# Kernel optimization log

Hardware: AMD Instinct MI355X
Metric: run time of the kernel (lower is better)

## Reference

```python
import jax, jax.numpy as jnp
import numpy as np

DIM = 256
QK = 256
HEADS = 8
NWIN = 16
TOPK = 4
MLP_RATIO = 4
SCALE = QK ** -0.5


def setup_inputs() -> dict:
    key = jax.random.key(0)
    ks = jax.random.split(key, 8)
    p = lambda k, shp: jax.random.normal(k, shp, jnp.float32) * 0.02
    hid = MLP_RATIO * DIM
    return {
        "x": jax.random.normal(ks[0], (8, DIM, 64, 64), jnp.float32),
        # to_q / to_kv : 1x1 Conv2d_BN (eval-mode BN with running stats 0/1 -> scale+shift)
        "wq": p(ks[1], (QK, DIM)), "gq": jnp.ones((QK,), jnp.float32), "bq": jnp.zeros((QK,), jnp.float32),
        "wkv": p(ks[2], (QK + DIM, DIM)), "gkv": jnp.ones((QK + DIM,), jnp.float32), "bkv": jnp.zeros((QK + DIM,), jnp.float32),
        # LEPE depthwise 5x5 conv
        "w_lepe": p(ks[3], (DIM, 1, 5, 5)), "b_lepe": jnp.zeros((DIM,), jnp.float32),
        # Mlp: fc1(1x1 Conv2d_BN) -> dwconv3x3 -> ReLU -> fc2(1x1 Conv2d_BN)
        "w_fc1": p(ks[4], (hid, DIM)), "g_fc1": jnp.ones((hid,), jnp.float32), "b_fc1": jnp.zeros((hid,), jnp.float32),
        "w_dw": p(ks[5], (hid, 1, 3, 3)), "b_dw": jnp.zeros((hid,), jnp.float32),
        "w_fc2": p(ks[6], (DIM, hid)), "g_fc2": jnp.ones((DIM,), jnp.float32), "b_fc2": jnp.zeros((DIM,), jnp.float32),
    }


def _dwconv(x, w, b, pad):
    # x: NCHW, w: (C,1,k,k) depthwise
    out = jax.lax.conv_general_dilated(
        x, w, (1, 1), [(pad, pad), (pad, pad)],
        feature_group_count=x.shape[1],
        dimension_numbers=("NCHW", "OIHW", "NCHW"))
    return out + b[None, :, None, None]


def _bra(x, wq, gq, bq, wkv, gkv, bkv, w_lepe, b_lepe):
    # Bi-Level Routing Attention. x: NCHW
    N, C, H, W = x.shape
    j = i = NWIN
    h, w_ = H // j, W // i          # per-window spatial (4,4)
    p2, w2 = j * i, h * w_          # 256 windows, 16 tokens/window
    xh = x.transpose(0, 2, 3, 1)    # NHWC
    # windowize: (N, p2, h, w, C)
    xw = xh.reshape(N, j, h, i, w_, C).transpose(0, 1, 3, 2, 4, 5).reshape(N, p2, h, w_, C)
    # 1x1 conv + BN(eval: stats 0/1) == matmul * gamma + beta
    q = (xw @ wq.T) * gq + bq                    # (N,p2,h,w,QK)
    kv = (xw @ wkv.T) * gkv + bkv                # (N,p2,h,w,QK+C)
    q_pix = q.reshape(N, p2, w2, QK)
    kv_pix = kv.reshape(N, p2, w2, QK + C)       # identity kv_down
    q_win = q.mean((2, 3))                       # (N,p2,QK)
    k_win = kv[..., :QK].mean((2, 3))            # (N,p2,QK)
    # LEPE on V in full-image layout
    v_img = kv[..., QK:].reshape(N, j, i, h, w_, C).transpose(0, 1, 3, 2, 4, 5).reshape(N, H, W, C)
    lepe = _dwconv(v_img.transpose(0, 3, 1, 2), w_lepe, b_lepe, 2).transpose(0, 2, 3, 1)  # NHWC
    # window-level topk routing (detached, non-differentiable)
    qd = jax.lax.stop_gradient(q_win)
    kd = jax.lax.stop_gradient(k_win)
    logit = (qd * SCALE) @ kd.transpose(0, 2, 1)            # (N,p2,p2)
    _, r_idx = jax.lax.top_k(logit, TOPK)                   # (N,p2,TOPK); r_weight unused (mul_weight='none')
    # gather selected KV windows: (N,p2,TOPK,w2,QK+C)
    kv_sel = jax.vmap(lambda kvp, idx: kvp[idx])(kv_pix, r_idx)
    ch_k, ch_v = QK // HEADS, C // HEADS
    k_sel = kv_sel[..., :QK].reshape(N, p2, TOPK * w2, HEADS, ch_k).transpose(0, 1, 3, 2, 4)
    v_sel = kv_sel[..., QK:].reshape(N, p2, TOPK * w2, HEADS, ch_v).transpose(0, 1, 3, 2, 4)
    qh = q_pix.reshape(N, p2, w2, HEADS, ch_k).transpose(0, 1, 3, 2, 4)
    attn = jax.nn.softmax(jnp.einsum("npmqc,npmkc->npmqk", qh * SCALE, k_sel), axis=-1)
    out = jnp.einsum("npmqk,npmkc->npmqc", attn, v_sel)     # (N,p2,HEADS,w2,ch_v)
    out = out.transpose(0, 1, 3, 2, 4).reshape(N, j, i, h, w_, C)
    out = out.transpose(0, 1, 3, 2, 4, 5).reshape(N, H, W, C)
    out = out + lepe                                         # wo = Identity
    return out.transpose(0, 3, 1, 2)                         # NCHW


def reference(x, wq, gq, bq, wkv, gkv, bkv, w_lepe, b_lepe,
              w_fc1, g_fc1, b_fc1, w_dw, b_dw, w_fc2, g_fc2, b_fc2):
    # top_Block: x = x + attn(x); x = x + mlp(x)   (drop_path inactive in eval)
    x = x + _bra(x, wq, gq, bq, wkv, gkv, bkv, w_lepe, b_lepe)
    h1 = jnp.einsum("nchw,dc->ndhw", x, w_fc1) * g_fc1[None, :, None, None] + b_fc1[None, :, None, None]
    h1 = jax.nn.relu(_dwconv(h1, w_dw, b_dw, 1))
    h2 = jnp.einsum("nchw,dc->ndhw", h1, w_fc2) * g_fc2[None, :, None, None] + b_fc2[None, :, None, None]
    return x + h2
```

## Files before the change

kernel.cpp:

```cpp
#include <hip/hip_runtime.h>
#include <hip/hip_bf16.h>

#define NBATCH 8
#define CDIM 256
#define HH 64
#define WW 64
#define HWSZ 4096
#define TT 32768
#define QKVD 768
#define TOPK 4
#define HID 1024
#define ATTN_SCALE 0.0625f

typedef __hip_bfloat16 bf16;
typedef __attribute__((ext_vector_type(8))) short s8v;
typedef __attribute__((ext_vector_type(4))) float f4v;

__device__ __forceinline__ float toF(bf16 v) { return __bfloat162float(v); }
__device__ __forceinline__ bf16  toB(float v) { return __float2bfloat16(v); }

__device__ __forceinline__ void gload_lds16(const bf16* g, bf16* l) {
    __builtin_amdgcn_global_load_lds(
        (const __attribute__((address_space(1))) void*)g,
        (__attribute__((address_space(3))) void*)l, 16, 0, 0);
}

__global__ void k_prep(const float* __restrict__ wq, const float* __restrict__ gq,
                       const float* __restrict__ wkv, const float* __restrict__ gkv,
                       const float* __restrict__ wfc1, const float* __restrict__ gfc1,
                       const float* __restrict__ wfc2, const float* __restrict__ gfc2,
                       const float* __restrict__ bq, const float* __restrict__ bkv,
                       const float* __restrict__ w_dw, const float* __restrict__ b_dw,
                       bf16* __restrict__ wbqkv, bf16* __restrict__ wbfc1,
                       bf16* __restrict__ wbfc2, float* __restrict__ bias768,
                       float* __restrict__ wdwT) {
    int i = blockIdx.x * 256 + threadIdx.x;
    if (i < 196608) {
        int r = i >> 8;
        float g = (r < 256) ? gq[r] : gkv[r - 256];
        float w = (r < 256) ? wq[i] : wkv[i - 65536];
        wbqkv[i] = toB(w * g);
        if (i < 768) bias768[i] = (i < 256) ? bq[i] : bkv[i - 256];
    } else if (i < 458752) {
        int j = i - 196608;
        wbfc1[j] = toB(wfc1[j] * gfc1[j >> 8]);
    } else if (i < 720896) {
        int j = i - 458752;
        wbfc2[j] = toB(wfc2[j] * gfc2[j >> 10]);
    } else if (i < 731136) {
        int j = i - 720896;
        int cg = j / 80, r = j - cg * 80;
        wdwT[j] = (r < 72) ? w_dw[(cg * 8 + (r & 7)) * 9 + (r >> 3)]
                           : b_dw[cg * 8 + (r - 72)];
    }
}

__global__ void k_xt(const float* __restrict__ x, bf16* __restrict__ xt) {
    __shared__ float tile[32][33];
    int s0 = blockIdx.x * 32, c0 = blockIdx.y * 32, n = blockIdx.z;
    int tx = threadIdx.x, ty = threadIdx.y;
#pragma unroll
    for (int r = 0; r < 4; r++)
        tile[ty + r * 8][tx] = x[(size_t)n * CDIM * HWSZ + (size_t)(c0 + ty + r * 8) * HWSZ + s0 + tx];
    __syncthreads();
#pragma unroll
    for (int r = 0; r < 4; r++)
        xt[((size_t)n * HWSZ + s0 + ty + r * 8) * CDIM + c0 + tx] = toB(tile[tx][ty + r * 8]);
}

__global__ void k_xwin(const float* __restrict__ x, float* __restrict__ xwin) {
    int b = blockIdx.x;
    int n = b >> 8, c = b & 255;
    int p = threadIdx.x, wy = p >> 4, wx = p & 15;
    const float* pl = x + ((size_t)n * CDIM + c) * HWSZ;
    float s = 0.f;
#pragma unroll
    for (int dy = 0; dy < 4; dy++)
#pragma unroll
        for (int dx = 0; dx < 4; dx++)
            s += pl[(wy * 4 + dy) * WW + wx * 4 + dx];
    xwin[((size_t)(n << 8) + p) * 256 + c] = s * 0.0625f;
}

__global__ void k_qkwin(const float* __restrict__ xwin,
                        const float* __restrict__ wq, const float* __restrict__ wkv,
                        const float* __restrict__ gq, const float* __restrict__ bq,
                        const float* __restrict__ gkv, const float* __restrict__ bkv,
                        float* __restrict__ qkwin) {
    __shared__ float As[16][68];
    __shared__ float Bs[16][68];
    int m0 = blockIdx.x * 64, n0 = blockIdx.y * 64;
    int tid = threadIdx.x;
    int tx = tid & 15, ty = tid >> 4;
    float acc[4][4] = {};
    for (int k0 = 0; k0 < 256; k0 += 16) {
#pragma unroll
        for (int r = 0; r < 4; r++) {
            int lin = tid + r * 256;
            int row = lin >> 4, kk = lin & 15;
            As[kk][row] = xwin[(size_t)(m0 + row) * 256 + k0 + kk];
            int n = n0 + row;
            const float* wr = (n < 256) ? (wq + (size_t)n * 256) : (wkv + (size_t)(n - 256) * 256);
            Bs[kk][row] = wr[k0 + kk];
        }
        __syncthreads();
#pragma unroll
        for (int kk = 0; kk < 16; kk++) {
            float a[4], bb[4];
#pragma unroll
            for (int i = 0; i < 4; i++) a[i] = As[kk][tx * 4 + i];
#pragma unroll
            for (int j = 0; j < 4; j++) bb[j] = Bs[kk][ty * 4 + j];
#pragma unroll
            for (int i = 0; i < 4; i++)
#pragma unroll
                for (int j = 0; j < 4; j++) acc[i][j] += a[i] * bb[j];
        }
        __syncthreads();
    }
#pragma unroll
    for (int j = 0; j < 4; j++) {
        int n = n0 + ty * 4 + j;
        float gg = (n < 256) ? gq[n] : gkv[n - 256];
        float bb = (n < 256) ? bq[n] : bkv[n - 256];
#pragma unroll
        for (int i = 0; i < 4; i++)
            qkwin[(size_t)(m0 + tx * 4 + i) * 512 + n] = acc[i][j] * gg + bb;
    }
}

__global__ void k_logits(const float* __restrict__ qkwin, float* __restrict__ logits) {
    __shared__ float As[16][68];
    __shared__ float Bs[16][68];
    int m0 = blockIdx.x * 64, n0 = blockIdx.y * 64, img = blockIdx.z;
    const float* base = qkwin + (size_t)(img << 8) * 512;
    int tid = threadIdx.x;
    int tx = tid & 15, ty = tid >> 4;
    float acc[4][4] = {};
    for (int k0 = 0; k0 < 256; k0 += 16) {
#pragma unroll
        for (int r = 0; r < 4; r++) {
            int lin = tid + r * 256;
            int row = lin >> 4, kk = lin & 15;
            As[kk][row] = base[(size_t)(m0 + row) * 512 + k0 + kk];
            Bs[kk][row] = base[(size_t)(n0 + row) * 512 + 256 + k0 + kk];
        }
        __syncthreads();
#pragma unroll
        for (int kk = 0; kk < 16; kk++) {
            float a[4], bb[4];
#pragma unroll
            for (int i = 0; i < 4; i++) a[i] = As[kk][tx * 4 + i];
#pragma unroll
            for (int j = 0; j < 4; j++) bb[j] = Bs[kk][ty * 4 + j];
#pragma unroll
            for (int i = 0; i < 4; i++)
#pragma unroll
                for (int j = 0; j < 4; j++) acc[i][j] += a[i] * bb[j];
        }
        __syncthreads();
    }
    float* Lr = logits + (size_t)(img << 8) * 256;
#pragma unroll
    for (int j = 0; j < 4; j++)
#pragma unroll
        for (int i = 0; i < 4; i++)
            Lr[(size_t)(m0 + tx * 4 + i) * 256 + n0 + ty * 4 + j] = acc[i][j];
}

__global__ __launch_bounds__(256) void k_topk(const float* __restrict__ logits,
                                              int* __restrict__ topk) {
    int row = blockIdx.x * 4 + (threadIdx.x >> 6);
    int lane = threadIdx.x & 63;
    float4 v4 = *(const float4*)(logits + (size_t)row * 256 + lane * 4);
    float v[4] = {v4.x, v4.y, v4.z, v4.w};
#pragma unroll
    for (int sel = 0; sel < TOPK; sel++) {
        float mv = v[0]; int mi = lane * 4;
#pragma unroll
        for (int j = 1; j < 4; j++)
            if (v[j] > mv) { mv = v[j]; mi = lane * 4 + j; }
#pragma unroll
        for (int off = 1; off < 64; off <<= 1) {
            float ov = __shfl_xor(mv, off);
            int oi = __shfl_xor(mi, off);
            if (ov > mv || (ov == mv && oi < mi)) { mv = ov; mi = oi; }
        }
        if (lane == 0) topk[(size_t)row * TOPK + sel] = mi;
        if ((mi >> 2) == lane) v[mi & 3] = -INFINITY;
    }
}

template <int BM, int BN>
__global__ __launch_bounds__(256) void k_mfma(const bf16* __restrict__ A,
                                              const bf16* __restrict__ Wb,
                                              const float* __restrict__ bias,
                                              bf16* __restrict__ out,
                                              int M, int N, int K) {
    constexpr int WROWS = BM / 2, WCOLS = BN / 2;
    constexpr int WM = WROWS / 16, WN = WCOLS / 16;
    constexpr int CA = (BM * 4) / 256;
    constexpr int CB = (BN * 4) / 256;
    __shared__ bf16 As[BM * 32];
    __shared__ bf16 Bs[BN * 32];
    int gx = gridDim.x;
    int lin = blockIdx.x + blockIdx.y * gx;
    int tot = gx * gridDim.y;
    int cpx = tot >> 3;
    int swz = (lin & 7) * cpx + (lin >> 3);
    int m0 = (swz % gx) * BM, n0 = (swz / gx) * BN;
    int tid = threadIdx.x;
    int w = tid >> 6, lane = tid & 63;
    int wr = w >> 1, wc = w & 1;
    int lm = lane & 15, lq = lane >> 4;
    f4v acc[WM][WN];
#pragma unroll
    for (int i = 0; i < WM; i++)
#pragma unroll
        for (int j = 0; j < WN; j++) acc[i][j] = (f4v){0.f, 0.f, 0.f, 0.f};

    for (int k0 = 0; k0 < K; k0 += 32) {
#pragma unroll
        for (int q = 0; q < CA; q++) {
            int c = tid + q * 256, row = c >> 2, col = c & 3;
            gload_lds16(A + (size_t)(m0 + row) * K + k0 + col * 8,
                        As + (size_t)(w * 64 + q * 256) * 8);
        }
#pragma unroll
        for (int q = 0; q < CB; q++) {
            int c = tid + q * 256, row = c >> 2, col = c & 3;
            gload_lds16(Wb + (size_t)(n0 + row) * K + k0 + col * 8,
                        Bs + (size_t)(w * 64 + q * 256) * 8);
        }
        asm volatile("s_waitcnt vmcnt(0)" ::: "memory");
        __syncthreads();
        s8v af[WM], bfr[WN];
#pragma unroll
        for (int i = 0; i < WM; i++)
            af[i] = *(const s8v*)&As[(wr * WROWS + i * 16 + lm) * 32 + lq * 8];
#pragma unroll
        for (int j = 0; j < WN; j++)
            bfr[j] = *(const s8v*)&Bs[(wc * WCOLS + j * 16 + lm) * 32 + lq * 8];
#pragma unroll
        for (int i = 0; i < WM; i++)
#pragma unroll
            for (int j = 0; j < WN; j++)
                acc[i][j] = __builtin_amdgcn_mfma_f32_16x16x32_bf16(af[i], bfr[j], acc[i][j], 0, 0, 0);
        __syncthreads();
    }
#pragma unroll
    for (int j = 0; j < WN; j++) {
        int n = n0 + wc * WCOLS + j * 16 + lm;
        float bb = bias[n];
#pragma unroll
        for (int i = 0; i < WM; i++) {
            int mb = m0 + wr * WROWS + i * 16 + lq * 4;
#pragma unroll
            for (int r = 0; r < 4; r++)
                out[(size_t)(mb + r) * N + n] = toB(acc[i][j][r] + bb);
        }
    }
}

__global__ __launch_bounds__(256) void k_lepe_t(const bf16* __restrict__ qkv,
                                                const float* __restrict__ w_lepe,
                                                const float* __restrict__ b_lepe,
                                                bf16* __restrict__ lepe) {
    __shared__ float lw[25 * 64 * 4];
    int tid = threadIdx.x;
    int cg = tid & 63;
    int slot = tid >> 6;
    int b = blockIdx.x;
    int n = b & 7;
    int bx = b >> 3;
    int y = bx >> 1;
    int x0 = (bx & 1) * 32 + slot * 8;
#pragma unroll
    for (int j = 0; j < 25; j++) {
        int g = tid + j * 256;
        float val = w_lepe[g];
        int ch = g / 25, k = g - ch * 25;
        lw[(k * 64 + (ch >> 2)) * 4 + (ch & 3)] = val;
    }
    float4 b4 = *(const float4*)(b_lepe + cg * 4);
    const float* bias4 = (const float*)&b4;
    __syncthreads();
    const bf16* vb = qkv + (size_t)n * HWSZ * QKVD + 512;
    bf16* dst = lepe + (size_t)n * HWSZ * CDIM;
    float o[8][4];
#pragma unroll
    for (int xi = 0; xi < 8; xi++)
#pragma unroll
        for (int c = 0; c < 4; c++) o[xi][c] = bias4[c];
#pragma unroll
    for (int dy = -2; dy <= 2; dy++) {
        int yy = y + dy;
        if (yy < 0 || yy >= HH) continue;
        float rf[12][4];
#pragma unroll
        for (int ii = 0; ii < 12; ii++) {
            int xx = x0 - 2 + ii;
            if (xx >= 0 && xx < WW) {
                uint2 v = *(const uint2*)(vb + (size_t)(yy * WW + xx) * QKVD + cg * 4);
                const bf16* pv = (const bf16*)&v;
#pragma unroll
                for (int c = 0; c < 4; c++) rf[ii][c] = toF(pv[c]);
            } else {
#pragma unroll
                for (int c = 0; c < 4; c++) rf[ii][c] = 0.f;
            }
        }
#pragma unroll
        for (int dx = 0; dx < 5; dx++) {
            int k = (dy + 2) * 5 + dx;
            float4 w4v = *(const float4*)&lw[(k * 64 + cg) * 4];
            const float* w4 = (const float*)&w4v;
#pragma unroll
            for (int xi = 0; xi < 8; xi++)
#pragma unroll
                for (int c = 0; c < 4; c++) o[xi][c] += rf[xi + dx][c] * w4[c];
        }
    }
#pragma unroll
    for (int xi = 0; xi < 8; xi++) {
        uint2 pk;
        bf16* pb = (bf16*)&pk;
#pragma unroll
        for (int c = 0; c < 4; c++) pb[c] = toB(o[xi][c]);
        *(uint2*)(dst + (size_t)(y * WW + x0 + xi) * CDIM + cg * 4) = pk;
    }
}

__global__ __launch_bounds__(256) void k_attn(const bf16* __restrict__ qkv,
                                              const int* __restrict__ topk,
                                              const bf16* __restrict__ lepe,
                                              bf16* x1t) {
    __shared__ bf16 vst[256][72];
    __shared__ bf16 plds[4][16][72];
    __shared__ float lsm[4][16];
    __shared__ int toks[64];
    int b = blockIdx.x;
    int n = b & 7, p = b >> 3;
    int wy = p >> 4, wx = p & 15;
    int tid = threadIdx.x;
    if (tid < 64) {
        int rp = topk[((size_t)(n << 8) + p) * TOPK + (tid >> 4)] & 255;
        int st = tid & 15;
        toks[tid] = ((rp >> 4) * 4 + (st >> 2)) * WW + (rp & 15) * 4 + (st & 3);
    }
    __syncthreads();
    const bf16* qbase = qkv + (size_t)n * HWSZ * QKVD;
    {
        int kt = tid & 63, jj = tid >> 6;
#pragma unroll
        for (int pass = 0; pass < 8; pass++) {
            int d0 = pass * 32 + jj * 8;
            uint4 v = *(const uint4*)(qbase + (size_t)toks[kt] * QKVD + 512 + d0);
            const bf16* pv = (const bf16*)&v;
#pragma unroll
            for (int e = 0; e < 8; e++) vst[d0 + e][kt] = pv[e];
        }
    }
    __syncthreads();
    int w = tid >> 6, lane = tid & 63;
    int ln = lane & 15, lq = lane >> 4;
    int myS = (wy * 4 + (ln >> 2)) * WW + wx * 4 + (ln & 3);
    const f4v fz = {0.f, 0.f, 0.f, 0.f};
    for (int hh = 0; hh < 2; hh++) {
        int h = w * 2 + hh;
        s8v qf = *(const s8v*)(qbase + (size_t)myS * QKVD + h * 32 + lq * 8);
        f4v st4[4];
#pragma unroll
        for (int t = 0; t < 4; t++) {
            s8v kf = *(const s8v*)(qbase + (size_t)toks[t * 16 + ln] * QKVD + 256 + h * 32 + lq * 8);
            st4[t] = __builtin_amdgcn_mfma_f32_16x16x32_bf16(kf, qf, fz, 0, 0, 0);
        }
        float mx = -INFINITY;
#pragma unroll
        for (int t = 0; t < 4; t++)
#pragma unroll
            for (int r = 0; r < 4; r++) mx = fmaxf(mx, st4[t][r]);
        mx = fmaxf(mx, __shfl_xor(mx, 16));
        mx = fmaxf(mx, __shfl_xor(mx, 32));
        mx *= ATTN_SCALE;
        float sum = 0.f;
#pragma unroll
        for (int t = 0; t < 4; t++)
#pragma unroll
            for (int r = 0; r < 4; r++) {
                float pp = __expf(st4[t][r] * ATTN_SCALE - mx);
                sum += pp;
                plds[w][ln][t * 16 + lq * 4 + r] = toB(pp);
            }
        sum += __shfl_xor(sum, 16);
        sum += __shfl_xor(sum, 32);
        if (lq == 0) lsm[w][ln] = sum;
        __syncthreads();
        s8v ap0 = *(const s8v*)&plds[w][ln][lq * 8];
        s8v ap1 = *(const s8v*)&plds[w][ln][32 + lq * 8];
#pragma unroll
        for (int dt = 0; dt < 2; dt++) {
            int dim = h * 32 + dt * 16 + ln;
            s8v vv0 = *(const s8v*)&vst[dim][lq * 8];
            s8v vv1 = *(const s8v*)&vst[dim][32 + lq * 8];
            f4v o = __builtin_amdgcn_mfma_f32_16x16x32_bf16(ap0, vv0, fz, 0, 0, 0);
            o = __builtin_amdgcn_mfma_f32_16x16x32_bf16(ap1, vv1, o, 0, 0, 0);
#pragma unroll
            for (int r = 0; r < 4; r++) {
                int t = lq * 4 + r;
                float linv = 1.f / lsm[w][t];
                int s = (wy * 4 + (t >> 2)) * WW + wx * 4 + (t & 3);
                size_t idx = ((size_t)n * HWSZ + s) * CDIM + dim;
                x1t[idx] = toB(o[r] * linv + toF(x1t[idx]) + toF(lepe[idx]));
            }
        }
        __syncthreads();
    }
}

__global__ __launch_bounds__(256) void k_dw3_t(const bf16* __restrict__ h1,
                                               const float* __restrict__ wdwT,
                                               bf16* __restrict__ h1p) {
    __shared__ float lw[64 * 81];
    int tid = threadIdx.x;
    int lin = blockIdx.x;
    int img = lin & 7;
    int rest = lin >> 3;
    int chalf = rest & 1;
    int seg = rest >> 1;
    int y = seg >> 1;
    int xh = seg & 1;
#pragma unroll
    for (int j = 0; j < 20; j++) {
        int g = tid + j * 256;
        int cgg = g / 80, r = g - cgg * 80;
        lw[cgg * 81 + r] = wdwT[chalf * 5120 + g];
    }
    __syncthreads();
    int cgl = tid & 63;
    int slot = tid >> 6;
    int cg = chalf * 64 + cgl;
    int x0 = xh * 32 + slot * 8;
    const float* wl = lw + cgl * 81;
    float o[8][8];
    {
        float4 b0 = *(const float4*)&wl[72];
        float4 b1 = *(const float4*)&wl[76];
        const float* p0 = (const float*)&b0;
        const float* p1 = (const float*)&b1;
#pragma unroll
        for (int xi = 0; xi < 8; xi++)
#pragma unroll
            for (int c = 0; c < 4; c++) { o[xi][c] = p0[c]; o[xi][c + 4] = p1[c]; }
    }
    const uint4* src = (const uint4*)h1 + (size_t)img * HWSZ * 128;
    uint4* dst = (uint4*)h1p + (size_t)img * HWSZ * 128;
#pragma unroll
    for (int dy = -1; dy <= 1; dy++) {
        int yy = y + dy;
        if (yy < 0 || yy >= HH) continue;
        float rf[10][8];
#pragma unroll
        for (int ii = 0; ii < 10; ii++) {
            int xx = x0 - 1 + ii;
            if (xx >= 0 && xx < WW) {
                uint4 v = src[(size_t)(yy * WW + xx) * 128 + cg];
                const bf16* pv = (const bf16*)&v;
#pragma unroll
                for (int c = 0; c < 8; c++) rf[ii][c] = toF(pv[c]);
            } else {
#pragma unroll
                for (int c = 0; c < 8; c++) rf[ii][c] = 0.f;
            }
        }
#pragma unroll
        for (int dx = 0; dx < 3; dx++) {
            int k = (dy + 1) * 3 + dx;
            float4 w0 = *(const float4*)&wl[k * 8];
            float4 w1 = *(const float4*)&wl[k * 8 + 4];
            const float* pw0 = (const float*)&w0;
            const float* pw1 = (const float*)&w1;
#pragma unroll
            for (int xi = 0; xi < 8; xi++)
#pragma unroll
                for (int c = 0; c < 4; c++) {
                    o[xi][c]     += rf[xi + dx][c]     * pw0[c];
                    o[xi][c + 4] += rf[xi + dx][c + 4] * pw1[c];
                }
        }
    }
#pragma unroll
    for (int xi = 0; xi < 8; xi++) {
        uint4 pk;
        bf16* pb = (bf16*)&pk;
#pragma unroll
        for (int c = 0; c < 8; c++) pb[c] = toB(fmaxf(o[xi][c], 0.f));
        dst[(size_t)(y * WW + x0 + xi) * 128 + cg] = pk;
    }
}

__global__ void k_final(const bf16* __restrict__ x1, const bf16* __restrict__ h2,
                        float* __restrict__ out) {
    __shared__ float tile[32][33];
    int s0 = blockIdx.x * 32, c0 = blockIdx.y * 32, n = blockIdx.z;
    int tx = threadIdx.x, ty = threadIdx.y;
#pragma unroll
    for (int r = 0; r < 4; r++) {
        int s = s0 + ty + r * 8;
        size_t idx = ((size_t)n * HWSZ + s) * CDIM + c0 + tx;
        tile[tx][ty + r * 8] = toF(x1[idx]) + toF(h2[idx]);
    }
    __syncthreads();
#pragma unroll
    for (int r = 0; r < 4; r++) {
        int c = c0 + ty + r * 8;
        out[(size_t)n * CDIM * HWSZ + (size_t)c * HWSZ + s0 + tx] = tile[ty + r * 8][tx];
    }
}

extern "C" void kernel_launch(void* const* d_in, const int* in_sizes, int n_in,
                              void* d_out, int out_size, void* d_ws, size_t ws_size,
                              hipStream_t stream) {
    (void)in_sizes; (void)n_in; (void)out_size; (void)ws_size;
    const float* x      = (const float*)d_in[0];
    const float* wq     = (const float*)d_in[1];
    const float* gq     = (const float*)d_in[2];
    const float* bq     = (const float*)d_in[3];
    const float* wkv    = (const float*)d_in[4];
    const float* gkv    = (const float*)d_in[5];
    const float* bkv    = (const float*)d_in[6];
    const float* w_lepe = (const float*)d_in[7];
    const float* b_lepe = (const float*)d_in[8];
    const float* w_fc1  = (const float*)d_in[9];
    const float* g_fc1  = (const float*)d_in[10];
    const float* b_fc1  = (const float*)d_in[11];
    const float* w_dw   = (const float*)d_in[12];
    const float* b_dw   = (const float*)d_in[13];
    const float* w_fc2  = (const float*)d_in[14];
    const float* g_fc2  = (const float*)d_in[15];
    const float* b_fc2  = (const float*)d_in[16];

    char* ws = (char*)d_ws;
    bf16*  qkv    = (bf16*)(ws);
    bf16*  lepe   = (bf16*)(ws + 50331648);
    bf16*  xt     = (bf16*)(ws + 67108864);
    bf16*  x1     = (bf16*)(ws + 67108864);
    bf16*  h1     = (bf16*)(ws + 83886080);
    bf16*  h1p    = (bf16*)(ws + 150994944);
    bf16*  h2     = (bf16*)(ws + 218103808);
    float* xwin   = (float*)(ws + 234881024);
    float* qkwin  = (float*)(ws + 236978176);
    float* logits = (float*)(ws + 241172480);
    int*   tk     = (int*)(ws + 243269632);
    bf16*  wbqkv  = (bf16*)(ws + 243302400);
    bf16*  wbfc1  = (bf16*)(ws + 243695616);
    bf16*  wbfc2  = (bf16*)(ws + 244219904);
    float* bias768= (float*)(ws + 244744192);
    float* wdwT   = (float*)(ws + 244747264);

    k_prep<<<2856, 256, 0, stream>>>(wq, gq, wkv, gkv, w_fc1, g_fc1, w_fc2, g_fc2,
                                     bq, bkv, w_dw, b_dw,
                                     wbqkv, wbfc1, wbfc2, bias768, wdwT);
    k_xt<<<dim3(128, 8, 8), dim3(32, 8), 0, stream>>>(x, xt);
    k_xwin<<<2048, 256, 0, stream>>>(x, xwin);
    k_qkwin<<<dim3(32, 8), 256, 0, stream>>>(xwin, wq, wkv, gq, bq, gkv, bkv, qkwin);
    k_logits<<<dim3(4, 4, 8), 256, 0, stream>>>(qkwin, logits);
    k_topk<<<512, 256, 0, stream>>>(logits, tk);
    k_mfma<128, 128><<<dim3(256, 6), 256, 0, stream>>>(
        xt, wbqkv, bias768, qkv, TT, QKVD, CDIM);
    k_lepe_t<<<1024, 256, 0, stream>>>(qkv, w_lepe, b_lepe, lepe);
    k_attn<<<2048, 256, 0, stream>>>(qkv, tk, lepe, x1);
    k_mfma<128, 128><<<dim3(256, 8), 256, 0, stream>>>(
        x1, wbfc1, b_fc1, h1, TT, HID, CDIM);
    k_dw3_t<<<2048, 256, 0, stream>>>(h1, wdwT, h1p);
    k_mfma<64, 128><<<dim3(512, 2), 256, 0, stream>>>(
        h1p, wbfc2, b_fc2, h2, TT, CDIM, HID);
    k_final<<<dim3(128, 8, 8), dim3(32, 8), 0, stream>>>(x1, h2, (float*)d_out);
}
```

Measured before the change: 395.7 us.

## Double-buffer LDS tiles in MFMA GEMM to overlap global loads with compute

The GEMM kernel now keeps two LDS buffers for A and B. It issues the global-to-LDS loads for the next K tile before running the MFMAs on the current tile, and needs only one barrier per iteration instead of two. This is meant to hide global load latency behind the matrix math. It doubles the LDS footprint, which may lower occupancy, and it relies on the ds_read ordering being correct before the next overwrite.

```diff
diff --git a/kernel.cpp b/kernel.cpp
--- a/kernel.cpp
+++ b/kernel.cpp
@@ -201,8 +201,8 @@
     constexpr int WM = WROWS / 16, WN = WCOLS / 16;
     constexpr int CA = (BM * 4) / 256;
     constexpr int CB = (BN * 4) / 256;
-    __shared__ bf16 As[BM * 32];
-    __shared__ bf16 Bs[BN * 32];
+    __shared__ bf16 As[2][BM * 32];
+    __shared__ bf16 Bs[2][BN * 32];
     int gx = gridDim.x;
     int lin = blockIdx.x + blockIdx.y * gx;
     int tot = gx * gridDim.y;
@@ -219,34 +219,47 @@
 #pragma unroll
         for (int j = 0; j < WN; j++) acc[i][j] = (f4v){0.f, 0.f, 0.f, 0.f};
 
-    for (int k0 = 0; k0 < K; k0 += 32) {
+    auto stage = [&](int buf, int k0) {
 #pragma unroll
         for (int q = 0; q < CA; q++) {
             int c = tid + q * 256, row = c >> 2, col = c & 3;
             gload_lds16(A + (size_t)(m0 + row) * K + k0 + col * 8,
-                        As + (size_t)(w * 64 + q * 256) * 8);
+                        As[buf] + (size_t)(w * 64 + q * 256) * 8);
         }
 #pragma unroll
         for (int q = 0; q < CB; q++) {
             int c = tid + q * 256, row = c >> 2, col = c & 3;
             gload_lds16(Wb + (size_t)(n0 + row) * K + k0 + col * 8,
-                        Bs + (size_t)(w * 64 + q * 256) * 8);
-        }
-        asm volatile("s_waitcnt vmcnt(0)" ::: "memory");
-        __syncthreads();
+                        Bs[buf] + (size_t)(w * 64 + q * 256) * 8);
+        }
+    };
+
+    const int NT = K / 32;
+    stage(0, 0);
+    asm volatile("s_waitcnt vmcnt(0)" ::: "memory");
+    __builtin_amdgcn_s_barrier();
+    __builtin_amdgcn_sched_barrier(0);
+    int cur = 0;
+    for (int t = 0; t < NT; t++) {
+        if (t + 1 < NT) stage(cur ^ 1, (t + 1) * 32);
         s8v af[WM], bfr[WN];
 #pragma unroll
         for (int i = 0; i < WM; i++)
-            af[i] = *(const s8v*)&As[(wr * WROWS + i * 16 + lm) * 32 + lq * 8];
+            af[i] = *(const s8v*)&As[cur][(wr * WROWS + i * 16 + lm) * 32 + lq * 8];
 #pragma unroll
         for (int j = 0; j < WN; j++)
-            bfr[j] = *(const s8v*)&Bs[(wc * WCOLS + j * 16 + lm) * 32 + lq * 8];
+            bfr[j] = *(const s8v*)&Bs[cur][(wc * WCOLS + j * 16 + lm) * 32 + lq * 8];
 #pragma unroll
         for (int i = 0; i < WM; i++)
 #pragma unroll
             for (int j = 0; j < WN; j++)
                 acc[i][j] = __builtin_amdgcn_mfma_f32_16x16x32_bf16(af[i], bfr[j], acc[i][j], 0, 0, 0);
-        __syncthreads();
+        if (t + 1 < NT) {
+            asm volatile("s_waitcnt vmcnt(0)" ::: "memory");
+            __builtin_amdgcn_s_barrier();
+            __builtin_amdgcn_sched_barrier(0);
+            cur ^= 1;
+        }
     }
 #pragma unroll
     for (int j = 0; j < WN; j++) {
```

After: 386.7 us. 2.3% less time.
